# Optimization experiments

Measured on AMD Instinct MI355X. Metric: run time of the kernel, lower is better.

Reference implementation:

```python
import jax, jax.numpy as jnp
import numpy as np

N = 8192
E = 262144
IN_DIM = 128
HID = 64


def setup_inputs() -> dict:
    key = jax.random.key(0)
    k1, k2, k3, k4 = jax.random.split(key, 4)
    x = jax.random.normal(k1, (N, IN_DIM), dtype=jnp.float32)
    edge_index = jax.random.randint(k2, (2, E), 0, N, dtype=jnp.int64)
    W1 = jax.random.normal(k3, (IN_DIM, HID), dtype=jnp.float32) / np.sqrt(IN_DIM)
    b1 = jnp.zeros((HID,), dtype=jnp.float32)
    W2 = jax.random.normal(k4, (HID, HID), dtype=jnp.float32) / np.sqrt(HID)
    b2 = jnp.zeros((HID,), dtype=jnp.float32)
    return {"x": x, "edge_index": edge_index, "W1": W1, "b1": b1, "W2": W2, "b2": b2}


def gcn_conv(x, src, dst, W, b):
    # PyG GCNConv: add self-loops, symmetric deg^{-1/2} normalization,
    # linear transform, scatter-add aggregation, bias.
    loop = jnp.arange(N, dtype=src.dtype)
    s = jnp.concatenate([src, loop])
    d = jnp.concatenate([dst, loop])
    deg = jax.ops.segment_sum(jnp.ones_like(d, dtype=x.dtype), d, num_segments=N)
    dinv = jnp.where(deg > 0, jax.lax.rsqrt(deg), 0.0)
    norm = dinv[s] * dinv[d]  # [E+N]
    h = x @ W                 # [N, out]
    out = jax.ops.segment_sum(h[s] * norm[:, None], d, num_segments=N)
    return out + b


def reference(x, edge_index, W1, b1, W2, b2):
    src, dst = edge_index[0], edge_index[1]
    h = jax.nn.relu(gcn_conv(x, src, dst, W1, b1))
    h = jax.nn.relu(gcn_conv(h, src, dst, W2, b2))
    sim = h @ h.T  # [N, N]
    return jax.nn.sigmoid(sim)
```

## Files before the change

kernel.cpp:

```cpp
#include <hip/hip_runtime.h>
#include <hip/hip_bf16.h>

#define N_NODES 8192
#define HID 64

typedef __attribute__((ext_vector_type(8))) short bf16x8;
typedef __attribute__((ext_vector_type(4))) float f32x4;

__global__ void k_deg_init(int* __restrict__ deg) {
    int i = blockIdx.x * 256 + threadIdx.x;
    deg[i] = 1;
}

__global__ void k_deg_count(const int* __restrict__ dst, int* __restrict__ deg, int E) {
    int e = blockIdx.x * 256 + threadIdx.x;
    if (e < E) atomicAdd(&deg[dst[e]], 1);
}

__global__ void k_dinv_inplace(int* __restrict__ degdinv) {
    int i = blockIdx.x * 256 + threadIdx.x;
    float d = (float)degdinv[i];
    ((float*)degdinv)[i] = rsqrtf(d);
}

__global__ void __launch_bounds__(1024) k_scan(const int* __restrict__ deg,
                                               int* __restrict__ off,
                                               int* __restrict__ cursor) {
    __shared__ int s[1024];
    const int t = threadIdx.x;
    int v[8];
    int sum = 0;
    const int base = t * 8;
#pragma unroll
    for (int j = 0; j < 8; ++j) { v[j] = deg[base + j] - 1; sum += v[j]; }
    s[t] = sum;
    __syncthreads();
    for (int d = 1; d < 1024; d <<= 1) {
        int x = (t >= d) ? s[t - d] : 0;
        __syncthreads();
        s[t] += x;
        __syncthreads();
    }
    int ex = s[t] - sum;
#pragma unroll
    for (int j = 0; j < 8; ++j) {
        off[base + j] = ex;
        cursor[base + j] = ex;
        ex += v[j];
    }
}

__global__ void k_fill(const int* __restrict__ src, const int* __restrict__ dst,
                       int* __restrict__ cursor, int* __restrict__ csr, int E) {
    int e = blockIdx.x * 256 + threadIdx.x;
    if (e >= E) return;
    int pos = atomicAdd(&cursor[dst[e]], 1);
    csr[pos] = src[e];
}

__global__ void __launch_bounds__(256) k_gemm(const float* __restrict__ X,
                                              const float* __restrict__ W,
                                              const float* __restrict__ dinv,
                                              float* __restrict__ Y, int K) {
    const int col  = threadIdx.x & 63;
    const int wv   = threadIdx.x >> 6;
    const int row0 = blockIdx.x * 16 + wv * 4;
    float a0 = 0.f, a1 = 0.f, a2 = 0.f, a3 = 0.f;
    const float* x0 = X + (size_t)row0 * K;
    for (int k = 0; k < K; ++k) {
        float w = W[k * 64 + col];
        a0 += x0[k] * w;
        a1 += x0[K + k] * w;
        a2 += x0[2 * K + k] * w;
        a3 += x0[3 * K + k] * w;
    }
    size_t o = (size_t)row0 * 64 + col;
    Y[o]       = a0 * dinv[row0];
    Y[o + 64]  = a1 * dinv[row0 + 1];
    Y[o + 128] = a2 * dinv[row0 + 2];
    Y[o + 192] = a3 * dinv[row0 + 3];
}

template <int MODE>
__global__ void __launch_bounds__(256) k_gather(const float* __restrict__ Hs,
                                                const float* __restrict__ dinv,
                                                const int* __restrict__ off,
                                                const int* __restrict__ csr,
                                                const float* __restrict__ bias,
                                                float* __restrict__ outf,
                                                __hip_bfloat16* __restrict__ outb,
                                                int E) {
    const int node = blockIdx.x * 4 + (threadIdx.x >> 6);
    const int lane = threadIdx.x & 63;
    float acc = Hs[(size_t)node * 64 + lane];
    int k = off[node];
    const int end = (node == N_NODES - 1) ? E : off[node + 1];
    for (; k + 1 < end; k += 2) {
        int s0 = csr[k];
        int s1 = csr[k + 1];
        float h0 = Hs[(size_t)s0 * 64 + lane];
        float h1 = Hs[(size_t)s1 * 64 + lane];
        acc += h0;
        acc += h1;
    }
    if (k < end) acc += Hs[(size_t)csr[k] * 64 + lane];
    float v = dinv[node] * acc + bias[lane];
    v = v > 0.f ? v : 0.f;
    if (MODE == 0) outf[(size_t)node * 64 + lane] = v;
    else           outb[(size_t)node * 64 + lane] = __float2bfloat16(v);
}

__global__ void __launch_bounds__(256) k_sim(const short* __restrict__ Hb,
                                             float* __restrict__ out) {
    __shared__ float lds[64][132];
    const int lane = threadIdx.x & 63;
    const int wv   = threadIdx.x >> 6;
    const int rh   = wv >> 1;
    const int ch   = wv & 1;
    const int br = blockIdx.y * 128 + rh * 64;
    const int bc = blockIdx.x * 128 + ch * 64;
    const int lr = lane & 15;
    const int kg = lane >> 4;

    bf16x8 a[4][2], b[4][2];
#pragma unroll
    for (int t = 0; t < 4; ++t)
#pragma unroll
        for (int kk = 0; kk < 2; ++kk) {
            a[t][kk] = *(const bf16x8*)(Hb + (size_t)(br + t * 16 + lr) * 64 + kk * 32 + kg * 8);
            b[t][kk] = *(const bf16x8*)(Hb + (size_t)(bc + t * 16 + lr) * 64 + kk * 32 + kg * 8);
        }

    f32x4 acc[4][4] = {};
#pragma unroll
    for (int i = 0; i < 4; ++i)
#pragma unroll
        for (int j = 0; j < 4; ++j) {
            acc[i][j] = __builtin_amdgcn_mfma_f32_16x16x32_bf16(a[i][0], b[j][0], acc[i][j], 0, 0, 0);
            acc[i][j] = __builtin_amdgcn_mfma_f32_16x16x32_bf16(a[i][1], b[j][1], acc[i][j], 0, 0, 0);
        }

#pragma unroll
    for (int i = 0; i < 4; ++i)
#pragma unroll
        for (int j = 0; j < 4; ++j)
#pragma unroll
            for (int r = 0; r < 4; ++r)
                acc[i][j][r] = 1.0f / (1.0f + __expf(-acc[i][j][r]));

    const int orow = threadIdx.x >> 5;
    const int oq   = threadIdx.x & 31;
    const size_t ocol = (size_t)blockIdx.x * 128 + oq * 4;
#pragma unroll
    for (int h = 0; h < 2; ++h) {
        if (rh == h) {
#pragma unroll
            for (int i = 0; i < 4; ++i)
#pragma unroll
                for (int j = 0; j < 4; ++j)
#pragma unroll
                    for (int r = 0; r < 4; ++r)
                        lds[i * 16 + kg * 4 + r][ch * 64 + j * 16 + lr] = acc[i][j][r];
        }
        __syncthreads();
#pragma unroll
        for (int p = 0; p < 8; ++p) {
            int rr = p * 8 + orow;
            f32x4 v = *(const f32x4*)&lds[rr][oq * 4];
            *(f32x4*)&out[(size_t)(blockIdx.y * 128 + h * 64 + rr) * N_NODES + ocol] = v;
        }
        __syncthreads();
    }
}

extern "C" void kernel_launch(void* const* d_in, const int* in_sizes, int n_in,
                              void* d_out, int out_size, void* d_ws, size_t ws_size,
                              hipStream_t stream) {
    const float* x  = (const float*)d_in[0];
    const int*   ei = (const int*)d_in[1];
    const float* W1 = (const float*)d_in[2];
    const float* b1 = (const float*)d_in[3];
    const float* W2 = (const float*)d_in[4];
    const float* b2 = (const float*)d_in[5];
    const int E = in_sizes[1] / 2;
    const int* src = ei;
    const int* dst = ei + E;

    char* ws = (char*)d_ws;
    int*   degdinv = (int*)ws;
    float* dinv    = (float*)ws;
    int*   off     = (int*)(ws + 32 * 1024);
    int*   csr     = (int*)(ws + 64 * 1024);
    float* A       = (float*)(ws + 64 * 1024 + 1024 * 1024);
    int*   cursor  = (int*)A;
    float* B       = (float*)(ws + 64 * 1024 + 3 * 1024 * 1024);
    __hip_bfloat16* h2b = (__hip_bfloat16*)B;

    const int NB = N_NODES / 256;
    const int EB = (E + 255) / 256;
    const int GB = N_NODES / 4;

    k_deg_init<<<NB, 256, 0, stream>>>(degdinv);
    k_deg_count<<<EB, 256, 0, stream>>>(dst, degdinv, E);
    k_scan<<<1, 1024, 0, stream>>>(degdinv, off, cursor);
    k_dinv_inplace<<<NB, 256, 0, stream>>>(degdinv);
    k_fill<<<EB, 256, 0, stream>>>(src, dst, cursor, csr, E);

    k_gemm<<<N_NODES / 16, 256, 0, stream>>>(x, W1, dinv, A, 128);
    k_gather<0><<<GB, 256, 0, stream>>>(A, dinv, off, csr, b1, B, nullptr, E);

    k_gemm<<<N_NODES / 16, 256, 0, stream>>>(B, W2, dinv, A, 64);
    k_gather<1><<<GB, 256, 0, stream>>>(A, dinv, off, csr, b2, nullptr, h2b, E);

    dim3 g(N_NODES / 128, N_NODES / 128);
    k_sim<<<g, 256, 0, stream>>>((const short*)h2b, (float*)d_out);
}
```

Baseline: 413.3 us.

## Fuse layer-2 GEMM into layer-1 gather and fold dinv into scan

The second GCN linear transform now runs inside the first aggregation kernel: each wavefront broadcasts its aggregated row with shuffles and multiplies it by W2 directly, which removes one GEMM launch and one round trip of the hidden matrix through memory. The degree-init kernel is replaced by a memset and the rsqrt normalization moves into the scan kernel, cutting two small launches. The total work is unchanged; only launch count and intermediate traffic drop. The fused per-node matvec reads W2 from global memory once per node and adds 64 shuffles per node.

```diff
diff --git a/kernel.cpp b/kernel.cpp
--- a/kernel.cpp
+++ b/kernel.cpp
@@ -6,24 +6,13 @@
 
 typedef __attribute__((ext_vector_type(8))) short bf16x8;
 typedef __attribute__((ext_vector_type(4))) float f32x4;
-
-__global__ void k_deg_init(int* __restrict__ deg) {
-    int i = blockIdx.x * 256 + threadIdx.x;
-    deg[i] = 1;
-}
 
 __global__ void k_deg_count(const int* __restrict__ dst, int* __restrict__ deg, int E) {
     int e = blockIdx.x * 256 + threadIdx.x;
     if (e < E) atomicAdd(&deg[dst[e]], 1);
 }
 
-__global__ void k_dinv_inplace(int* __restrict__ degdinv) {
-    int i = blockIdx.x * 256 + threadIdx.x;
-    float d = (float)degdinv[i];
-    ((float*)degdinv)[i] = rsqrtf(d);
-}
-
-__global__ void __launch_bounds__(1024) k_scan(const int* __restrict__ deg,
+__global__ void __launch_bounds__(1024) k_scan(int* __restrict__ degdinv,
                                                int* __restrict__ off,
                                                int* __restrict__ cursor) {
     __shared__ int s[1024];
@@ -32,7 +21,7 @@
     int sum = 0;
     const int base = t * 8;
 #pragma unroll
-    for (int j = 0; j < 8; ++j) { v[j] = deg[base + j] - 1; sum += v[j]; }
+    for (int j = 0; j < 8; ++j) { v[j] = degdinv[base + j]; sum += v[j]; }
     s[t] = sum;
     __syncthreads();
     for (int d = 1; d < 1024; d <<= 1) {
@@ -47,6 +36,7 @@
         off[base + j] = ex;
         cursor[base + j] = ex;
         ex += v[j];
+        ((float*)degdinv)[base + j] = rsqrtf((float)(v[j] + 1));
     }
 }
 
@@ -81,15 +71,48 @@
     Y[o + 192] = a3 * dinv[row0 + 3];
 }
 
-template <int MODE>
-__global__ void __launch_bounds__(256) k_gather(const float* __restrict__ Hs,
-                                                const float* __restrict__ dinv,
-                                                const int* __restrict__ off,
-                                                const int* __restrict__ csr,
-                                                const float* __restrict__ bias,
-                                                float* __restrict__ outf,
-                                                __hip_bfloat16* __restrict__ outb,
-                                                int E) {
+__global__ void __launch_bounds__(256) k_gather_gemm2(const float* __restrict__ Hs1,
+                                                      const float* __restrict__ dinv,
+                                                      const int* __restrict__ off,
+                                                      const int* __restrict__ csr,
+                                                      const float* __restrict__ b1,
+                                                      const float* __restrict__ W2,
+                                                      float* __restrict__ Hs2,
+                                                      int E) {
+    const int node = blockIdx.x * 4 + (threadIdx.x >> 6);
+    const int lane = threadIdx.x & 63;
+    float acc = Hs1[(size_t)node * 64 + lane];
+    int k = off[node];
+    const int end = (node == N_NODES - 1) ? E : off[node + 1];
+    for (; k + 1 < end; k += 2) {
+        int s0 = csr[k];
+        int s1 = csr[k + 1];
+        float h0 = Hs1[(size_t)s0 * 64 + lane];
+        float h1 = Hs1[(size_t)s1 * 64 + lane];
+        acc += h0;
+        acc += h1;
+    }
+    if (k < end) acc += Hs1[(size_t)csr[k] * 64 + lane];
+    const float di = dinv[node];
+    float h1v = di * acc + b1[lane];
+    h1v = h1v > 0.f ? h1v : 0.f;
+
+    float o = 0.f;
+#pragma unroll
+    for (int kk = 0; kk < HID; ++kk) {
+        float hk = __shfl(h1v, kk, 64);
+        o += hk * W2[kk * 64 + lane];
+    }
+    Hs2[(size_t)node * 64 + lane] = o * di;
+}
+
+__global__ void __launch_bounds__(256) k_gather2(const float* __restrict__ Hs,
+                                                 const float* __restrict__ dinv,
+                                                 const int* __restrict__ off,
+                                                 const int* __restrict__ csr,
+                                                 const float* __restrict__ bias,
+                                                 __hip_bfloat16* __restrict__ outb,
+                                                 int E) {
     const int node = blockIdx.x * 4 + (threadIdx.x >> 6);
     const int lane = threadIdx.x & 63;
     float acc = Hs[(size_t)node * 64 + lane];
@@ -106,8 +129,7 @@
     if (k < end) acc += Hs[(size_t)csr[k] * 64 + lane];
     float v = dinv[node] * acc + bias[lane];
     v = v > 0.f ? v : 0.f;
-    if (MODE == 0) outf[(size_t)node * 64 + lane] = v;
-    else           outb[(size_t)node * 64 + lane] = __float2bfloat16(v);
+    outb[(size_t)node * 64 + lane] = __float2bfloat16(v);
 }
 
 __global__ void __launch_bounds__(256) k_sim(const short* __restrict__ Hb,
@@ -194,23 +216,20 @@
     float* A       = (float*)(ws + 64 * 1024 + 1024 * 1024);
     int*   cursor  = (int*)A;
     float* B       = (float*)(ws + 64 * 1024 + 3 * 1024 * 1024);
-    __hip_bfloat16* h2b = (__hip_bfloat16*)B;
-
-    const int NB = N_NODES / 256;
+    __hip_bfloat16* h2b = (__hip_bfloat16*)A;
+
     const int EB = (E + 255) / 256;
     const int GB = N_NODES / 4;
 
-    k_deg_init<<<NB, 256, 0, stream>>>(degdinv);
+    hipMemsetAsync(degdinv, 0, N_NODES * sizeof(int), stream);
     k_deg_count<<<EB, 256, 0, stream>>>(dst, degdinv, E);
     k_scan<<<1, 1024, 0, stream>>>(degdinv, off, cursor);
-    k_dinv_inplace<<<NB, 256, 0, stream>>>(degdinv);
     k_fill<<<EB, 256, 0, stream>>>(src, dst, cursor, csr, E);
 
     k_gemm<<<N_NODES / 16, 256, 0, stream>>>(x, W1, dinv, A, 128);
-    k_gather<0><<<GB, 256, 0, stream>>>(A, dinv, off, csr, b1, B, nullptr, E);
-
-    k_gemm<<<N_NODES / 16, 256, 0, stream>>>(B, W2, dinv, A, 64);
-    k_gather<1><<<GB, 256, 0, stream>>>(A, dinv, off, csr, b2, nullptr, h2b, E);
+    k_gather_gemm2<<<GB, 256, 0, stream>>>(A, dinv, off, csr, b1, W2, B, E);
+
+    k_gather2<<<GB, 256, 0, stream>>>(B, dinv, off, csr, b2, h2b, E);
 
     dim3 g(N_NODES / 128, N_NODES / 128);
     k_sim<<<g, 256, 0, stream>>>((const short*)h2b, (float*)d_out);
```

Measured after the change: 391.7 us. 1.06x faster.

## Fuse GCN preprocessing and both layers into one cooperative persistent kernel

Applied to the files above, without the earlier changes.

Replaces the nine small kernel launches (degree count, scan, CSR fill, two GEMMs, two gathers) with a single cooperative kernel that uses grid-wide syncs between phases. The first GEMM runs before the degree count, with normalization applied at gather time. The second GEMM is fused into the first gather through wavefront shuffles. This removes launch gaps and one intermediate round trip. In exchange the scan runs in a single block, grid syncs are added, and the grid size depends on an occupancy query.

```diff
diff --git a/kernel.cpp b/kernel.cpp
--- a/kernel.cpp
+++ b/kernel.cpp
@@ -1,5 +1,8 @@
 #include <hip/hip_runtime.h>
 #include <hip/hip_bf16.h>
+#include <hip/hip_cooperative_groups.h>
+
+namespace cg = cooperative_groups;
 
 #define N_NODES 8192
 #define HID 64
@@ -7,107 +10,107 @@
 typedef __attribute__((ext_vector_type(8))) short bf16x8;
 typedef __attribute__((ext_vector_type(4))) float f32x4;
 
-__global__ void k_deg_init(int* __restrict__ deg) {
-    int i = blockIdx.x * 256 + threadIdx.x;
-    deg[i] = 1;
-}
-
-__global__ void k_deg_count(const int* __restrict__ dst, int* __restrict__ deg, int E) {
-    int e = blockIdx.x * 256 + threadIdx.x;
-    if (e < E) atomicAdd(&deg[dst[e]], 1);
-}
-
-__global__ void k_dinv_inplace(int* __restrict__ degdinv) {
-    int i = blockIdx.x * 256 + threadIdx.x;
-    float d = (float)degdinv[i];
-    ((float*)degdinv)[i] = rsqrtf(d);
-}
-
-__global__ void __launch_bounds__(1024) k_scan(const int* __restrict__ deg,
-                                               int* __restrict__ off,
-                                               int* __restrict__ cursor) {
-    __shared__ int s[1024];
-    const int t = threadIdx.x;
-    int v[8];
-    int sum = 0;
-    const int base = t * 8;
-#pragma unroll
-    for (int j = 0; j < 8; ++j) { v[j] = deg[base + j] - 1; sum += v[j]; }
-    s[t] = sum;
-    __syncthreads();
-    for (int d = 1; d < 1024; d <<= 1) {
-        int x = (t >= d) ? s[t - d] : 0;
+__global__ void __launch_bounds__(256, 4) k_gnn(
+    const float* __restrict__ x, const int* __restrict__ src,
+    const int* __restrict__ dst, const float* __restrict__ W1,
+    const float* __restrict__ b1, const float* __restrict__ W2,
+    const float* __restrict__ b2, int* __restrict__ degdinv,
+    int* __restrict__ off, int* __restrict__ cursor, int* __restrict__ csr,
+    float* __restrict__ A, float* __restrict__ B,
+    __hip_bfloat16* __restrict__ h2b, int E)
+{
+    cg::grid_group grid = cg::this_grid();
+    const int tid  = threadIdx.x;
+    const int lane = tid & 63;
+    const int wv   = tid >> 6;
+    const int gtid = blockIdx.x * 256 + tid;
+    const int nthr = gridDim.x * 256;
+    const int gw   = blockIdx.x * 4 + wv;
+    const int nw   = gridDim.x * 4;
+
+    for (int i = gtid; i < N_NODES; i += nthr) degdinv[i] = 0;
+    for (int r = gw; r < N_NODES; r += nw) {
+        const float* xr = x + (size_t)r * 128;
+        float a = 0.f;
+#pragma unroll 8
+        for (int k = 0; k < 128; ++k) a += xr[k] * W1[k * 64 + lane];
+        A[(size_t)r * 64 + lane] = a;
+    }
+    grid.sync();
+
+    for (int e = gtid; e < E; e += nthr) atomicAdd(&degdinv[dst[e]], 1);
+    grid.sync();
+
+    if (blockIdx.x == 0) {
+        __shared__ int s[256];
+        int v[32];
+        int sum = 0;
+        const int base = tid * 32;
+#pragma unroll
+        for (int j = 0; j < 32; ++j) { v[j] = degdinv[base + j]; sum += v[j]; }
+        s[tid] = sum;
         __syncthreads();
-        s[t] += x;
-        __syncthreads();
-    }
-    int ex = s[t] - sum;
-#pragma unroll
-    for (int j = 0; j < 8; ++j) {
-        off[base + j] = ex;
-        cursor[base + j] = ex;
-        ex += v[j];
-    }
-}
-
-__global__ void k_fill(const int* __restrict__ src, const int* __restrict__ dst,
-                       int* __restrict__ cursor, int* __restrict__ csr, int E) {
-    int e = blockIdx.x * 256 + threadIdx.x;
-    if (e >= E) return;
-    int pos = atomicAdd(&cursor[dst[e]], 1);
-    csr[pos] = src[e];
-}
-
-__global__ void __launch_bounds__(256) k_gemm(const float* __restrict__ X,
-                                              const float* __restrict__ W,
-                                              const float* __restrict__ dinv,
-                                              float* __restrict__ Y, int K) {
-    const int col  = threadIdx.x & 63;
-    const int wv   = threadIdx.x >> 6;
-    const int row0 = blockIdx.x * 16 + wv * 4;
-    float a0 = 0.f, a1 = 0.f, a2 = 0.f, a3 = 0.f;
-    const float* x0 = X + (size_t)row0 * K;
-    for (int k = 0; k < K; ++k) {
-        float w = W[k * 64 + col];
-        a0 += x0[k] * w;
-        a1 += x0[K + k] * w;
-        a2 += x0[2 * K + k] * w;
-        a3 += x0[3 * K + k] * w;
-    }
-    size_t o = (size_t)row0 * 64 + col;
-    Y[o]       = a0 * dinv[row0];
-    Y[o + 64]  = a1 * dinv[row0 + 1];
-    Y[o + 128] = a2 * dinv[row0 + 2];
-    Y[o + 192] = a3 * dinv[row0 + 3];
-}
-
-template <int MODE>
-__global__ void __launch_bounds__(256) k_gather(const float* __restrict__ Hs,
-                                                const float* __restrict__ dinv,
-                                                const int* __restrict__ off,
-                                                const int* __restrict__ csr,
-                                                const float* __restrict__ bias,
-                                                float* __restrict__ outf,
-                                                __hip_bfloat16* __restrict__ outb,
-                                                int E) {
-    const int node = blockIdx.x * 4 + (threadIdx.x >> 6);
-    const int lane = threadIdx.x & 63;
-    float acc = Hs[(size_t)node * 64 + lane];
-    int k = off[node];
-    const int end = (node == N_NODES - 1) ? E : off[node + 1];
-    for (; k + 1 < end; k += 2) {
-        int s0 = csr[k];
-        int s1 = csr[k + 1];
-        float h0 = Hs[(size_t)s0 * 64 + lane];
-        float h1 = Hs[(size_t)s1 * 64 + lane];
-        acc += h0;
-        acc += h1;
-    }
-    if (k < end) acc += Hs[(size_t)csr[k] * 64 + lane];
-    float v = dinv[node] * acc + bias[lane];
-    v = v > 0.f ? v : 0.f;
-    if (MODE == 0) outf[(size_t)node * 64 + lane] = v;
-    else           outb[(size_t)node * 64 + lane] = __float2bfloat16(v);
+        for (int d = 1; d < 256; d <<= 1) {
+            int xx = (tid >= d) ? s[tid - d] : 0;
+            __syncthreads();
+            s[tid] += xx;
+            __syncthreads();
+        }
+        int ex = s[tid] - sum;
+#pragma unroll
+        for (int j = 0; j < 32; ++j) {
+            off[base + j] = ex;
+            cursor[base + j] = ex;
+            ex += v[j];
+            ((float*)degdinv)[base + j] = rsqrtf((float)(v[j] + 1));
+        }
+    }
+    grid.sync();
+    const float* dinv = (const float*)degdinv;
+
+    for (int e = gtid; e < E; e += nthr) {
+        int pos = atomicAdd(&cursor[dst[e]], 1);
+        csr[pos] = src[e];
+    }
+    grid.sync();
+
+    for (int node = gw; node < N_NODES; node += nw) {
+        const float di = dinv[node];
+        float acc = A[(size_t)node * 64 + lane] * di;
+        int k = off[node];
+        const int end = (node == N_NODES - 1) ? E : off[node + 1];
+        for (; k + 1 < end; k += 2) {
+            int s0 = csr[k], s1 = csr[k + 1];
+            float h0 = A[(size_t)s0 * 64 + lane] * dinv[s0];
+            float h1 = A[(size_t)s1 * 64 + lane] * dinv[s1];
+            acc += h0;
+            acc += h1;
+        }
+        if (k < end) { int s0 = csr[k]; acc += A[(size_t)s0 * 64 + lane] * dinv[s0]; }
+        float h1v = di * acc + b1[lane];
+        h1v = h1v > 0.f ? h1v : 0.f;
+        float o = 0.f;
+#pragma unroll 8
+        for (int kk = 0; kk < HID; ++kk)
+            o += __shfl(h1v, kk, 64) * W2[kk * 64 + lane];
+        B[(size_t)node * 64 + lane] = o * di;
+    }
+    grid.sync();
+
+    for (int node = gw; node < N_NODES; node += nw) {
+        float acc = B[(size_t)node * 64 + lane];
+        int k = off[node];
+        const int end = (node == N_NODES - 1) ? E : off[node + 1];
+        for (; k + 1 < end; k += 2) {
+            int s0 = csr[k], s1 = csr[k + 1];
+            acc += B[(size_t)s0 * 64 + lane];
+            acc += B[(size_t)s1 * 64 + lane];
+        }
+        if (k < end) acc += B[(size_t)csr[k] * 64 + lane];
+        float v = dinv[node] * acc + b2[lane];
+        v = v > 0.f ? v : 0.f;
+        h2b[(size_t)node * 64 + lane] = __float2bfloat16(v);
+    }
 }
 
 __global__ void __launch_bounds__(256) k_sim(const short* __restrict__ Hb,
@@ -182,35 +185,30 @@
     const float* b1 = (const float*)d_in[3];
     const float* W2 = (const float*)d_in[4];
     const float* b2 = (const float*)d_in[5];
-    const int E = in_sizes[1] / 2;
+    int E = in_sizes[1] / 2;
     const int* src = ei;
     const int* dst = ei + E;
 
     char* ws = (char*)d_ws;
     int*   degdinv = (int*)ws;
-    float* dinv    = (float*)ws;
     int*   off     = (int*)(ws + 32 * 1024);
-    int*   csr     = (int*)(ws + 64 * 1024);
-    float* A       = (float*)(ws + 64 * 1024 + 1024 * 1024);
-    int*   cursor  = (int*)A;
-    float* B       = (float*)(ws + 64 * 1024 + 3 * 1024 * 1024);
-    __hip_bfloat16* h2b = (__hip_bfloat16*)B;
-
-    const int NB = N_NODES / 256;
-    const int EB = (E + 255) / 256;
-    const int GB = N_NODES / 4;
-
-    k_deg_init<<<NB, 256, 0, stream>>>(degdinv);
-    k_deg_count<<<EB, 256, 0, stream>>>(dst, degdinv, E);
-    k_scan<<<1, 1024, 0, stream>>>(degdinv, off, cursor);
-    k_dinv_inplace<<<NB, 256, 0, stream>>>(degdinv);
-    k_fill<<<EB, 256, 0, stream>>>(src, dst, cursor, csr, E);
-
-    k_gemm<<<N_NODES / 16, 256, 0, stream>>>(x, W1, dinv, A, 128);
-    k_gather<0><<<GB, 256, 0, stream>>>(A, dinv, off, csr, b1, B, nullptr, E);
-
-    k_gemm<<<N_NODES / 16, 256, 0, stream>>>(B, W2, dinv, A, 64);
-    k_gather<1><<<GB, 256, 0, stream>>>(A, dinv, off, csr, b2, nullptr, h2b, E);
+    int*   cursor  = (int*)(ws + 64 * 1024);
+    int*   csr     = (int*)(ws + 96 * 1024);
+    float* A       = (float*)(ws + 96 * 1024 + 1024 * 1024);
+    float* B       = (float*)(ws + 96 * 1024 + 3 * 1024 * 1024);
+    __hip_bfloat16* h2b = (__hip_bfloat16*)A;
+
+    int mb = 0;
+    hipOccupancyMaxActiveBlocksPerMultiprocessor(&mb, (const void*)k_gnn, 256, 0);
+    if (mb < 1) mb = 1;
+    int nb = mb * 256;
+    if (nb > 1024) nb = 1024;
+
+    void* kargs[] = {(void*)&x, (void*)&src, (void*)&dst, (void*)&W1, (void*)&b1,
+                     (void*)&W2, (void*)&b2, (void*)&degdinv, (void*)&off,
+                     (void*)&cursor, (void*)&csr, (void*)&A, (void*)&B,
+                     (void*)&h2b, (void*)&E};
+    hipLaunchCooperativeKernel((const void*)k_gnn, dim3(nb), dim3(256), kargs, 0, stream);
 
     dim3 g(N_NODES / 128, N_NODES / 128);
     k_sim<<<g, 256, 0, stream>>>((const short*)h2b, (float*)d_out);
```

Measured after the change: 904.6 us. +118.9%, slower.
